# Kernel tuning notes

Measured on AMD Instinct MI355X. Metric: run time of the kernel, lower is better.

Reference implementation:

```python
import jax, jax.numpy as jnp
import numpy as np

B, S, E, H, L = 4, 512, 768, 12, 12
D = E // H
FF = 4 * E
EPS = 1e-5
SCALE = jnp.float32(768.0 ** 0.5)  # emb_size ** (1/2), applied AFTER softmax per source


def setup_inputs() -> dict:
    key = jax.random.key(0)
    ks = jax.random.split(key, 18)
    std = 0.02
    n = lambda k, shp: (jax.random.normal(k, shp, jnp.float32) * std)
    return {
        "x": jax.random.normal(ks[0], (B, S, E), jnp.float32),
        "Wqkv": n(ks[1], (L, E, 3 * E)),
        "bqkv": n(ks[2], (L, 3 * E)),
        "Wp": n(ks[3], (L, E, E)),
        "bp": n(ks[4], (L, E)),
        "W1": n(ks[5], (L, E, FF)),
        "b1": n(ks[6], (L, FF)),
        "W2": n(ks[7], (L, FF, E)),
        "b2": n(ks[8], (L, E)),
        "ln1_g": jnp.ones((L, E), jnp.float32), "ln1_b": jnp.zeros((L, E), jnp.float32),
        "ln2_g": jnp.ones((L, E), jnp.float32), "ln2_b": jnp.zeros((L, E), jnp.float32),
        "ln3_g": jnp.ones((L, E), jnp.float32), "ln3_b": jnp.zeros((L, E), jnp.float32),
        "ln4_g": jnp.ones((L, E), jnp.float32), "ln4_b": jnp.zeros((L, E), jnp.float32),
    }


def _ln(x, g, b):
    m = jnp.mean(x, axis=-1, keepdims=True)
    v = jnp.mean(jnp.square(x - m), axis=-1, keepdims=True)
    return (x - m) * jax.lax.rsqrt(v + EPS) * g + b


def _block(x, p):
    Wqkv, bqkv, Wp, bp, W1, b1, W2, b2, g1, be1, g2, be2, g3, be3, g4, be4 = p
    # --- attention branch ---
    h = _ln(x, g1, be1)
    qkv = h @ Wqkv + bqkv                      # [B,S,3E]
    qkv = qkv.reshape(B, S, H, D, 3)           # qkv is innermost factor in source rearrange
    q = jnp.transpose(qkv[..., 0], (0, 2, 1, 3))  # [B,H,S,D]
    k = jnp.transpose(qkv[..., 1], (0, 2, 1, 3))
    v = jnp.transpose(qkv[..., 2], (0, 2, 1, 3))
    energy = jnp.einsum('bhqd,bhkd->bhqk', q, k)
    att = jax.nn.softmax(energy, axis=-1) / SCALE  # NOTE: scaling AFTER softmax (faithful)
    o = jnp.einsum('bhqk,bhkd->bhqd', att, v)
    o = jnp.transpose(o, (0, 2, 1, 3)).reshape(B, S, E)
    o = o @ Wp + bp
    r1 = _ln(o, g2, be2) + x                   # first ResidualAdd (final LN inside branch)
    # --- feed-forward branch ---
    f = _ln(r1, g3, be3)
    f = jax.nn.gelu(f @ W1 + b1, approximate=False)
    f = f @ W2 + b2
    r2 = _ln(f, g4, be4) + r1                  # second ResidualAdd
    return x + r2                              # outer residual: x = x + block(x)


def reference(x, Wqkv, bqkv, Wp, bp, W1, b1, W2, b2,
              ln1_g, ln1_b, ln2_g, ln2_b, ln3_g, ln3_b, ln4_g, ln4_b):
    params = (Wqkv, bqkv, Wp, bp, W1, b1, W2, b2,
              ln1_g, ln1_b, ln2_g, ln2_b, ln3_g, ln3_b, ln4_g, ln4_b)
    out, _ = jax.lax.scan(lambda c, p: (_block(c, p), None), x, params)
    return out
```

## Files before the change

kernel.cpp:

```cpp
#include <hip/hip_runtime.h>
#include <hip/hip_bf16.h>
#include <stdint.h>

#define LAYERS 12
#define M_ROWS 2048
#define E_DIM 768
#define FF_DIM 3072
#define QKV_DIM 2304
#define SCALE_INV 0.036084391824351615f

typedef __hip_bfloat16 bf16;
typedef __attribute__((ext_vector_type(8))) __bf16 bf16x8;
typedef __attribute__((ext_vector_type(4))) float f32x4;

__device__ __forceinline__ float bf2f(bf16 v) { return __bfloat162float(v); }
__device__ __forceinline__ bf16 f2bf(float v) { return __float2bfloat16(v); }

__device__ __forceinline__ float gelu_f(float x) {
  return 0.5f * x * (1.0f + erff(x * 0.70710678118654752f));
}

__device__ __forceinline__ void async16(const bf16* g, bf16* l) {
  __builtin_amdgcn_global_load_lds(
      (const __attribute__((address_space(1))) void*)g,
      (__attribute__((address_space(3))) void*)l, 16, 0, 0);
}

__global__ __launch_bounds__(256) void transpose_k(
    const float* __restrict__ w0, const float* __restrict__ w1,
    const float* __restrict__ w2, const float* __restrict__ w3,
    bf16* __restrict__ t0, bf16* __restrict__ t1,
    bf16* __restrict__ t2, bf16* __restrict__ t3)
{
  __shared__ float T[32][33];
  int bid = blockIdx.x;
  const float* src; bf16* dst; int K, N, tile;
  if (bid < 1728)      { src = w0; dst = t0; K = 768;  N = 2304; tile = bid; }
  else if (bid < 2304) { src = w1; dst = t1; K = 768;  N = 768;  tile = bid - 1728; }
  else if (bid < 4608) { src = w2; dst = t2; K = 768;  N = 3072; tile = bid - 2304; }
  else                 { src = w3; dst = t3; K = 3072; N = 768;  tile = bid - 4608; }
  int tilesN = N >> 5;
  int tk = tile / tilesN;
  int tn = tile - tk * tilesN;
  int tx = threadIdx.x & 31, ty = threadIdx.x >> 5;
  int k0 = tk << 5, n0 = tn << 5;
#pragma unroll
  for (int i = 0; i < 4; i++)
    T[ty + i * 8][tx] = src[(size_t)(k0 + ty + i * 8) * N + n0 + tx];
  __syncthreads();
#pragma unroll
  for (int i = 0; i < 4; i++)
    dst[(size_t)(n0 + ty + i * 8) * K + k0 + tx] = f2bf(T[tx][ty + i * 8]);
}

template<int OUT_BF16, int NADD, int NPART>
__global__ __launch_bounds__(256) void ln_k(
    const float* __restrict__ in, const float* __restrict__ gamma,
    const float* __restrict__ beta, const float* __restrict__ add0,
    const float* __restrict__ add1, void* __restrict__ outp)
{
  int row = blockIdx.x, tid = threadIdx.x;
  size_t rb = (size_t)row * 768;
  float v[3]; float s = 0.f, sq = 0.f;
#pragma unroll
  for (int j = 0; j < 3; j++) {
    int c = tid + j * 256;
    float x = in[rb + c];
    if (NPART == 2) x += in[(size_t)M_ROWS * 768 + rb + c];
    v[j] = x;
    s += x; sq += x * x;
  }
#pragma unroll
  for (int off = 32; off; off >>= 1) {
    s += __shfl_xor(s, off);
    sq += __shfl_xor(sq, off);
  }
  __shared__ float red[8];
  int wv = tid >> 6;
  if ((tid & 63) == 0) { red[wv] = s; red[4 + wv] = sq; }
  __syncthreads();
  s  = red[0] + red[1] + red[2] + red[3];
  sq = red[4] + red[5] + red[6] + red[7];
  float mean = s * (1.0f / 768.0f);
  float var  = sq * (1.0f / 768.0f) - mean * mean;
  float rstd = rsqrtf(var + 1e-5f);
#pragma unroll
  for (int j = 0; j < 3; j++) {
    int c = tid + j * 256;
    float val = (v[j] - mean) * rstd * gamma[c] + beta[c];
    if (NADD >= 1) val += add0[rb + c];
    if (NADD >= 2) val += add1[rb + c];
    if (OUT_BF16) ((bf16*)outp)[rb + c] = f2bf(val);
    else          ((float*)outp)[rb + c] = val;
  }
}

template<int OUT_MODE, int NSPLIT>
__global__ __launch_bounds__(256) void gemm2_k(
    const bf16* __restrict__ A, const bf16* __restrict__ BT,
    const float* __restrict__ bias, void* __restrict__ Cout,
    bf16* __restrict__ qo, bf16* __restrict__ ko, bf16* __restrict__ vo,
    int N, int K)
{
  __shared__ __align__(16) bf16 Als[2][128 * 32];
  __shared__ __align__(16) bf16 Bls[2][64 * 32];
  int tid = threadIdx.x;
  int lane = tid & 63, w = tid >> 6;
  int l15 = lane & 15, l4 = lane >> 4;
  int Nt = N >> 6;
  int mt = blockIdx.x / Nt, ntile = blockIdx.x - mt * Nt;
  int m0 = mt << 7, n0 = ntile << 6;
  int sp = (NSPLIT > 1) ? blockIdx.y : 0;
  int Kc = K / NSPLIT;
  int kbeg = sp * Kc, kend = kbeg + Kc;
  const bf16* Ap = A + (size_t)m0 * K;
  const bf16* Bp = BT + (size_t)n0 * K;
  int ar = tid >> 2;
  int ac = (tid & 3) * 8;

  f32x4 acc[2][4] = {};

  async16(Ap + (size_t)ar * K + kbeg + ac,        &Als[0][w * 512]);
  async16(Ap + (size_t)(ar + 64) * K + kbeg + ac, &Als[0][2048 + w * 512]);
  async16(Bp + (size_t)ar * K + kbeg + ac,        &Bls[0][w * 512]);
  __syncthreads();

  int cur = 0;
  for (int k0 = kbeg; k0 < kend; k0 += 32) {
    if (k0 + 32 < kend) {
      int kn = k0 + 32;
      async16(Ap + (size_t)ar * K + kn + ac,        &Als[cur ^ 1][w * 512]);
      async16(Ap + (size_t)(ar + 64) * K + kn + ac, &Als[cur ^ 1][2048 + w * 512]);
      async16(Bp + (size_t)ar * K + kn + ac,        &Bls[cur ^ 1][w * 512]);
    }
    bf16x8 af[2], bfr[4];
#pragma unroll
    for (int i = 0; i < 2; i++)
      af[i] = *(const bf16x8*)&Als[cur][(w * 32 + i * 16 + l15) * 32 + l4 * 8];
#pragma unroll
    for (int j = 0; j < 4; j++)
      bfr[j] = *(const bf16x8*)&Bls[cur][(j * 16 + l15) * 32 + l4 * 8];
#pragma unroll
    for (int i = 0; i < 2; i++)
#pragma unroll
      for (int j = 0; j < 4; j++)
        acc[i][j] = __builtin_amdgcn_mfma_f32_16x16x32_bf16(af[i], bfr[j], acc[i][j], 0, 0, 0);
    __syncthreads();
    cur ^= 1;
  }

#pragma unroll
  for (int i = 0; i < 2; i++) {
    int mbase = m0 + w * 32 + i * 16 + (l4 << 2);
#pragma unroll
    for (int j = 0; j < 4; j++) {
      int n = n0 + j * 16 + l15;
      float bvs = (NSPLIT == 1 || sp == 0) ? bias[n] : 0.0f;
      if (OUT_MODE == 3) {
        int h = n / 192;
        int rm = n - h * 192;
        int d = rm / 3;
        int t = rm - d * 3;
#pragma unroll
        for (int rg = 0; rg < 4; rg++) {
          int m = mbase + rg;
          float val = acc[i][j][rg] + bvs;
          int b = m >> 9, sIdx = m & 511;
          int bh = b * 12 + h;
          if (t == 2)
            vo[(size_t)((bh << 6) + d) * 512 + sIdx] = f2bf(val);
          else {
            bf16* dsts = (t == 0) ? qo : ko;
            dsts[(size_t)((bh << 9) + sIdx) * 64 + d] = f2bf(val);
          }
        }
      } else {
#pragma unroll
        for (int rg = 0; rg < 4; rg++) {
          int m = mbase + rg;
          float val = acc[i][j][rg] + bvs;
          if (OUT_MODE == 0)
            ((float*)Cout)[(size_t)sp * M_ROWS * N + (size_t)m * N + n] = val;
          else if (OUT_MODE == 1)
            ((bf16*)Cout)[(size_t)m * N + n] = f2bf(val);
          else
            ((bf16*)Cout)[(size_t)m * N + n] = f2bf(gelu_f(val));
        }
      }
    }
  }
}

#define PSTR 80
__global__ __launch_bounds__(256) void attn_k(
    const bf16* __restrict__ q, const bf16* __restrict__ k,
    const bf16* __restrict__ vT, bf16* __restrict__ o)
{
  __shared__ __align__(16) bf16 Kls[64 * 64];
  __shared__ __align__(16) bf16 Vls[64 * 64];
  __shared__ __align__(16) bf16 Pls[4][16 * PSTR];
  int tid = threadIdx.x;
  int lane = tid & 63, w = tid >> 6;
  int l15 = lane & 15, l4 = lane >> 4;
  int qt = blockIdx.x & 7;
  int bh = blockIdx.x >> 3;
  size_t base = (size_t)bh * 32768;

  const bf16* qrowp = q + base + (size_t)(qt * 64 + w * 16 + l15) * 64 + l4 * 8;
  bf16x8 qf0 = *(const bf16x8*)qrowp;
  bf16x8 qf1 = *(const bf16x8*)(qrowp + 32);

  float mrow[4] = {-1e30f, -1e30f, -1e30f, -1e30f};
  float lsum[4] = {0.f, 0.f, 0.f, 0.f};
  f32x4 Oacc[4] = {};
  const f32x4 zed = {0.f, 0.f, 0.f, 0.f};
  bf16* pw = &Pls[w][0];

  for (int kt = 0; kt < 8; kt++) {
    __syncthreads();
#pragma unroll
    for (int rep = 0; rep < 2; rep++) {
      int c = tid + rep * 256;
      int row = c >> 3, col8 = (c & 7) * 8;
      *(uint4*)&Kls[row * 64 + col8] =
          *(const uint4*)(k + base + (size_t)(kt * 64 + row) * 64 + col8);
      *(uint4*)&Vls[row * 64 + col8] =
          *(const uint4*)(vT + base + (size_t)row * 512 + kt * 64 + col8);
    }
    __syncthreads();
    f32x4 e[4];
#pragma unroll
    for (int jt = 0; jt < 4; jt++) {
      bf16x8 kf0 = *(const bf16x8*)&Kls[(jt * 16 + l15) * 64 + l4 * 8];
      bf16x8 kf1 = *(const bf16x8*)&Kls[(jt * 16 + l15) * 64 + l4 * 8 + 32];
      e[jt] = __builtin_amdgcn_mfma_f32_16x16x32_bf16(qf0, kf0, zed, 0, 0, 0);
      e[jt] = __builtin_amdgcn_mfma_f32_16x16x32_bf16(qf1, kf1, e[jt], 0, 0, 0);
    }
    float al[4];
#pragma unroll
    for (int rg = 0; rg < 4; rg++) {
      float mn = fmaxf(fmaxf(e[0][rg], e[1][rg]), fmaxf(e[2][rg], e[3][rg]));
#pragma unroll
      for (int off = 1; off < 16; off <<= 1) mn = fmaxf(mn, __shfl_xor(mn, off));
      float mnew = fmaxf(mrow[rg], mn);
      al[rg] = __expf(mrow[rg] - mnew);
      mrow[rg] = mnew;
    }
    float rs[4] = {0.f, 0.f, 0.f, 0.f};
#pragma unroll
    for (int jt = 0; jt < 4; jt++)
#pragma unroll
      for (int rg = 0; rg < 4; rg++) {
        float p = __expf(e[jt][rg] - mrow[rg]);
        rs[rg] += p;
        pw[(l4 * 4 + rg) * PSTR + jt * 16 + l15] = f2bf(p);
      }
#pragma unroll
    for (int rg = 0; rg < 4; rg++) {
#pragma unroll
      for (int off = 1; off < 16; off <<= 1) rs[rg] += __shfl_xor(rs[rg], off);
      lsum[rg] = lsum[rg] * al[rg] + rs[rg];
    }
#pragma unroll
    for (int dt = 0; dt < 4; dt++)
#pragma unroll
      for (int rg = 0; rg < 4; rg++) Oacc[dt][rg] *= al[rg];
    bf16x8 pf0 = *(const bf16x8*)&pw[l15 * PSTR + l4 * 8];
    bf16x8 pf1 = *(const bf16x8*)&pw[l15 * PSTR + l4 * 8 + 32];
#pragma unroll
    for (int dt = 0; dt < 4; dt++) {
      bf16x8 vf0 = *(const bf16x8*)&Vls[(dt * 16 + l15) * 64 + l4 * 8];
      bf16x8 vf1 = *(const bf16x8*)&Vls[(dt * 16 + l15) * 64 + l4 * 8 + 32];
      Oacc[dt] = __builtin_amdgcn_mfma_f32_16x16x32_bf16(pf0, vf0, Oacc[dt], 0, 0, 0);
      Oacc[dt] = __builtin_amdgcn_mfma_f32_16x16x32_bf16(pf1, vf1, Oacc[dt], 0, 0, 0);
    }
  }
  int b = bh / 12, h = bh - b * 12;
#pragma unroll
  for (int rg = 0; rg < 4; rg++) {
    int qrow = qt * 64 + w * 16 + l4 * 4 + rg;
    float inv = SCALE_INV / lsum[rg];
    size_t rowoff = (size_t)(b * 512 + qrow) * 768 + h * 64;
#pragma unroll
    for (int dt = 0; dt < 4; dt++)
      o[rowoff + dt * 16 + l15] = f2bf(Oacc[dt][rg] * inv);
  }
}

extern "C" void kernel_launch(void* const* d_in, const int* in_sizes, int n_in,
                              void* d_out, int out_size, void* d_ws, size_t ws_size,
                              hipStream_t stream)
{
  const float* x    = (const float*)d_in[0];
  const float* Wqkv = (const float*)d_in[1];
  const float* bqkv = (const float*)d_in[2];
  const float* Wp   = (const float*)d_in[3];
  const float* bp   = (const float*)d_in[4];
  const float* W1   = (const float*)d_in[5];
  const float* b1   = (const float*)d_in[6];
  const float* W2   = (const float*)d_in[7];
  const float* b2   = (const float*)d_in[8];
  const float* g1  = (const float*)d_in[9];
  const float* be1 = (const float*)d_in[10];
  const float* g2  = (const float*)d_in[11];
  const float* be2 = (const float*)d_in[12];
  const float* g3  = (const float*)d_in[13];
  const float* be3 = (const float*)d_in[14];
  const float* g4  = (const float*)d_in[15];
  const float* be4 = (const float*)d_in[16];
  float* xout = (float*)d_out;

  char* ws = (char*)d_ws;
  size_t off = 0;
  auto alloc = [&](size_t bytes) -> char* {
    char* p = ws + off;
    off += (bytes + 255) & ~(size_t)255;
    return p;
  };
  const size_t NTOK = (size_t)M_ROWS * E_DIM;
  bf16*  qb  = (bf16*)alloc(NTOK * 2);
  bf16*  kb  = (bf16*)alloc(NTOK * 2);
  bf16*  vb  = (bf16*)alloc(NTOK * 2);
  bf16*  hb  = (bf16*)alloc(NTOK * 2);
  bf16*  ob  = (bf16*)alloc(NTOK * 2);
  bf16*  f1b = (bf16*)alloc((size_t)M_ROWS * FF_DIM * 2);
  float* tmp = (float*)alloc(NTOK * 4 * 2);
  float* r1  = (float*)alloc(NTOK * 4);
  bf16*  tq  = (bf16*)alloc((size_t)768 * 2304 * 2);
  bf16*  tp  = (bf16*)alloc((size_t)768 * 768 * 2);
  bf16*  t1  = (bf16*)alloc((size_t)768 * 3072 * 2);
  bf16*  t2  = (bf16*)alloc((size_t)3072 * 768 * 2);
  if (off > ws_size) {
    hipMemsetAsync(d_out, 0x7f, (size_t)out_size * 4, stream);
    return;
  }

  hipMemcpyAsync(d_out, x, (size_t)out_size * 4, hipMemcpyDeviceToDevice, stream);

  for (int l = 0; l < LAYERS; l++) {
    const float* wq  = Wqkv + (size_t)l * 768 * 2304;
    const float* wp_ = Wp   + (size_t)l * 768 * 768;
    const float* w1_ = W1   + (size_t)l * 768 * 3072;
    const float* w2_ = W2   + (size_t)l * 3072 * 768;

    transpose_k<<<6912, 256, 0, stream>>>(wq, wp_, w1_, w2_, tq, tp, t1, t2);

    ln_k<1, 0, 1><<<2048, 256, 0, stream>>>(xout, g1 + l * 768, be1 + l * 768,
                                            nullptr, nullptr, hb);
    gemm2_k<3, 1><<<dim3(16 * 36, 1), 256, 0, stream>>>(
        hb, tq, bqkv + (size_t)l * 2304, nullptr, qb, kb, vb, 2304, 768);
    attn_k<<<384, 256, 0, stream>>>(qb, kb, vb, ob);
    gemm2_k<0, 2><<<dim3(16 * 12, 2), 256, 0, stream>>>(
        ob, tp, bp + (size_t)l * 768, tmp, nullptr, nullptr, nullptr, 768, 768);
    ln_k<0, 1, 2><<<2048, 256, 0, stream>>>(tmp, g2 + l * 768, be2 + l * 768,
                                            xout, nullptr, r1);
    ln_k<1, 0, 1><<<2048, 256, 0, stream>>>(r1, g3 + l * 768, be3 + l * 768,
                                            nullptr, nullptr, hb);
    gemm2_k<2, 1><<<dim3(16 * 48, 1), 256, 0, stream>>>(
        hb, t1, b1 + (size_t)l * 3072, f1b, nullptr, nullptr, nullptr, 3072, 768);
    gemm2_k<0, 2><<<dim3(16 * 12, 2), 256, 0, stream>>>(
        f1b, t2, b2 + (size_t)l * 768, tmp, nullptr, nullptr, nullptr, 768, 3072);
    ln_k<0, 2, 2><<<2048, 256, 0, stream>>>(tmp, g4 + l * 768, be4 + l * 768,
                                            r1, xout, xout);
  }
}
```

Before: 1.984 ms.

## Use 128x128 GEMM tiles with XCD-aware block mapping and async attention loads

The GEMM tile grows from 128x64 to 128x128, so each wave computes a 64x64 sub-tile with 16 MFMA accumulators. This raises operand reuse per LDS load and halves the grid. Block indices are remapped so consecutive tiles land on the same XCD, which should improve L2 locality. The attention kernel now loads K/V tiles with global_load_lds async copies instead of register round-trips. The cost is fewer blocks: the Wp/W2 GEMMs get only 192 blocks, which may underfill the 256 CUs, and each thread needs more registers.

```diff
diff --git a/kernel.cpp b/kernel.cpp
--- a/kernel.cpp
+++ b/kernel.cpp
@@ -96,52 +96,62 @@
 }
 
 template<int OUT_MODE, int NSPLIT>
-__global__ __launch_bounds__(256) void gemm2_k(
+__global__ __launch_bounds__(256) void gemm3_k(
     const bf16* __restrict__ A, const bf16* __restrict__ BT,
     const float* __restrict__ bias, void* __restrict__ Cout,
     bf16* __restrict__ qo, bf16* __restrict__ ko, bf16* __restrict__ vo,
     int N, int K)
 {
   __shared__ __align__(16) bf16 Als[2][128 * 32];
-  __shared__ __align__(16) bf16 Bls[2][64 * 32];
+  __shared__ __align__(16) bf16 Bls[2][128 * 32];
   int tid = threadIdx.x;
   int lane = tid & 63, w = tid >> 6;
   int l15 = lane & 15, l4 = lane >> 4;
-  int Nt = N >> 6;
-  int mt = blockIdx.x / Nt, ntile = blockIdx.x - mt * Nt;
-  int m0 = mt << 7, n0 = ntile << 6;
+  int Nt = N >> 7;
+  int G = 16 * Nt;
+  int bid = blockIdx.x;
+  int xcd = bid & 7, jj = bid >> 3;
+  int g = xcd * (G >> 3) + jj;
+  int mt = g & 15, ntile = g >> 4;
+  int m0 = mt << 7, n0 = ntile << 7;
   int sp = (NSPLIT > 1) ? blockIdx.y : 0;
   int Kc = K / NSPLIT;
   int kbeg = sp * Kc, kend = kbeg + Kc;
-  const bf16* Ap = A + (size_t)m0 * K;
-  const bf16* Bp = BT + (size_t)n0 * K;
+  int wm = (w >> 1) * 64, wn = (w & 1) * 64;
   int ar = tid >> 2;
   int ac = (tid & 3) * 8;
 
-  f32x4 acc[2][4] = {};
-
-  async16(Ap + (size_t)ar * K + kbeg + ac,        &Als[0][w * 512]);
-  async16(Ap + (size_t)(ar + 64) * K + kbeg + ac, &Als[0][2048 + w * 512]);
-  async16(Bp + (size_t)ar * K + kbeg + ac,        &Bls[0][w * 512]);
+  const bf16* a0 = A + (size_t)(m0 + ar) * K + kbeg + ac;
+  const bf16* a1 = a0 + (size_t)64 * K;
+  const bf16* b0 = BT + (size_t)(n0 + ar) * K + kbeg + ac;
+  const bf16* b1 = b0 + (size_t)64 * K;
+
+  f32x4 acc[4][4] = {};
+
+  async16(a0, &Als[0][w * 512]);
+  async16(a1, &Als[0][2048 + w * 512]);
+  async16(b0, &Bls[0][w * 512]);
+  async16(b1, &Bls[0][2048 + w * 512]);
   __syncthreads();
 
   int cur = 0;
   for (int k0 = kbeg; k0 < kend; k0 += 32) {
     if (k0 + 32 < kend) {
-      int kn = k0 + 32;
-      async16(Ap + (size_t)ar * K + kn + ac,        &Als[cur ^ 1][w * 512]);
-      async16(Ap + (size_t)(ar + 64) * K + kn + ac, &Als[cur ^ 1][2048 + w * 512]);
-      async16(Bp + (size_t)ar * K + kn + ac,        &Bls[cur ^ 1][w * 512]);
-    }
-    bf16x8 af[2], bfr[4];
-#pragma unroll
-    for (int i = 0; i < 2; i++)
-      af[i] = *(const bf16x8*)&Als[cur][(w * 32 + i * 16 + l15) * 32 + l4 * 8];
+      a0 += 32; a1 += 32; b0 += 32; b1 += 32;
+      async16(a0, &Als[cur ^ 1][w * 512]);
+      async16(a1, &Als[cur ^ 1][2048 + w * 512]);
+      async16(b0, &Bls[cur ^ 1][w * 512]);
+      async16(b1, &Bls[cur ^ 1][2048 + w * 512]);
+    }
+    bf16x8 af[4], bfr[4];
+#pragma unroll
+    for (int i = 0; i < 4; i++)
+      af[i] = *(const bf16x8*)&Als[cur][(wm + i * 16 + l15) * 32 + l4 * 8];
 #pragma unroll
     for (int j = 0; j < 4; j++)
-      bfr[j] = *(const bf16x8*)&Bls[cur][(j * 16 + l15) * 32 + l4 * 8];
-#pragma unroll
-    for (int i = 0; i < 2; i++)
+      bfr[j] = *(const bf16x8*)&Bls[cur][(wn + j * 16 + l15) * 32 + l4 * 8];
+#pragma unroll
+    for (int i = 0; i < 4; i++)
 #pragma unroll
       for (int j = 0; j < 4; j++)
         acc[i][j] = __builtin_amdgcn_mfma_f32_16x16x32_bf16(af[i], bfr[j], acc[i][j], 0, 0, 0);
@@ -150,11 +160,11 @@
   }
 
 #pragma unroll
-  for (int i = 0; i < 2; i++) {
-    int mbase = m0 + w * 32 + i * 16 + (l4 << 2);
+  for (int i = 0; i < 4; i++) {
+    int mbase = m0 + wm + i * 16 + (l4 << 2);
 #pragma unroll
     for (int j = 0; j < 4; j++) {
-      int n = n0 + j * 16 + l15;
+      int n = n0 + wn + j * 16 + l15;
       float bvs = (NSPLIT == 1 || sp == 0) ? bias[n] : 0.0f;
       if (OUT_MODE == 3) {
         int h = n / 192;
@@ -210,6 +220,10 @@
   bf16x8 qf0 = *(const bf16x8*)qrowp;
   bf16x8 qf1 = *(const bf16x8*)(qrowp + 32);
 
+  int rr = tid >> 3, cc = (tid & 7) * 8;
+  const bf16* ksrc = k + base + (size_t)rr * 64 + cc;
+  const bf16* vsrc = vT + base + (size_t)rr * 512 + cc;
+
   float mrow[4] = {-1e30f, -1e30f, -1e30f, -1e30f};
   float lsum[4] = {0.f, 0.f, 0.f, 0.f};
   f32x4 Oacc[4] = {};
@@ -218,15 +232,10 @@
 
   for (int kt = 0; kt < 8; kt++) {
     __syncthreads();
-#pragma unroll
-    for (int rep = 0; rep < 2; rep++) {
-      int c = tid + rep * 256;
-      int row = c >> 3, col8 = (c & 7) * 8;
-      *(uint4*)&Kls[row * 64 + col8] =
-          *(const uint4*)(k + base + (size_t)(kt * 64 + row) * 64 + col8);
-      *(uint4*)&Vls[row * 64 + col8] =
-          *(const uint4*)(vT + base + (size_t)row * 512 + kt * 64 + col8);
-    }
+    async16(ksrc + (size_t)kt * 4096,        &Kls[w * 512]);
+    async16(ksrc + (size_t)kt * 4096 + 2048, &Kls[2048 + w * 512]);
+    async16(vsrc + kt * 64,                  &Vls[w * 512]);
+    async16(vsrc + kt * 64 + (size_t)32 * 512, &Vls[2048 + w * 512]);
     __syncthreads();
     f32x4 e[4];
 #pragma unroll
@@ -347,18 +356,18 @@
 
     ln_k<1, 0, 1><<<2048, 256, 0, stream>>>(xout, g1 + l * 768, be1 + l * 768,
                                             nullptr, nullptr, hb);
-    gemm2_k<3, 1><<<dim3(16 * 36, 1), 256, 0, stream>>>(
+    gemm3_k<3, 1><<<dim3(16 * 18, 1), 256, 0, stream>>>(
         hb, tq, bqkv + (size_t)l * 2304, nullptr, qb, kb, vb, 2304, 768);
     attn_k<<<384, 256, 0, stream>>>(qb, kb, vb, ob);
-    gemm2_k<0, 2><<<dim3(16 * 12, 2), 256, 0, stream>>>(
+    gemm3_k<0, 2><<<dim3(16 * 6, 2), 256, 0, stream>>>(
         ob, tp, bp + (size_t)l * 768, tmp, nullptr, nullptr, nullptr, 768, 768);
     ln_k<0, 1, 2><<<2048, 256, 0, stream>>>(tmp, g2 + l * 768, be2 + l * 768,
                                             xout, nullptr, r1);
     ln_k<1, 0, 1><<<2048, 256, 0, stream>>>(r1, g3 + l * 768, be3 + l * 768,
                                             nullptr, nullptr, hb);
-    gemm2_k<2, 1><<<dim3(16 * 48, 1), 256, 0, stream>>>(
+    gemm3_k<2, 1><<<dim3(16 * 24, 1), 256, 0, stream>>>(
         hb, t1, b1 + (size_t)l * 3072, f1b, nullptr, nullptr, nullptr, 3072, 768);
-    gemm2_k<0, 2><<<dim3(16 * 12, 2), 256, 0, stream>>>(
+    gemm3_k<0, 2><<<dim3(16 * 6, 2), 256, 0, stream>>>(
         f1b, t2, b2 + (size_t)l * 768, tmp, nullptr, nullptr, nullptr, 768, 3072);
     ln_k<0, 2, 2><<<2048, 256, 0, stream>>>(tmp, g4 + l * 768, be4 + l * 768,
                                             r1, xout, xout);
```

Result: slower. 2.195 ms (+10.6%).

## Hoist weight transposes out of layer loop, fuse adjacent LayerNorms, async attention loads

Applied to the files above, without the earlier changes.

Transposes and casts all layers' weights in a single launch up front instead of once per layer. Fuses the post-attention LayerNorm with the pre-FFN LayerNorm, and the final LayerNorm with the next layer's input LayerNorm, removing separate kernels and a re-read of the fp32 activations. Attention K/V tiles are loaded with direct global-to-LDS async loads instead of register round-trips. This uses a larger workspace for all transposed weights and relies on barriers to cover the async LDS writes.

```diff
diff --git a/kernel.cpp b/kernel.cpp
--- a/kernel.cpp
+++ b/kernel.cpp
@@ -26,19 +26,20 @@
       (__attribute__((address_space(3))) void*)l, 16, 0, 0);
 }
 
-__global__ __launch_bounds__(256) void transpose_k(
-    const float* __restrict__ w0, const float* __restrict__ w1,
-    const float* __restrict__ w2, const float* __restrict__ w3,
-    bf16* __restrict__ t0, bf16* __restrict__ t1,
-    bf16* __restrict__ t2, bf16* __restrict__ t3)
+__global__ __launch_bounds__(256) void transpose_all_k(
+    const float* __restrict__ Wqkv, const float* __restrict__ Wp,
+    const float* __restrict__ W1, const float* __restrict__ W2,
+    bf16* __restrict__ tq, bf16* __restrict__ tp,
+    bf16* __restrict__ t1, bf16* __restrict__ t2)
 {
   __shared__ float T[32][33];
+  int l = blockIdx.y;
   int bid = blockIdx.x;
   const float* src; bf16* dst; int K, N, tile;
-  if (bid < 1728)      { src = w0; dst = t0; K = 768;  N = 2304; tile = bid; }
-  else if (bid < 2304) { src = w1; dst = t1; K = 768;  N = 768;  tile = bid - 1728; }
-  else if (bid < 4608) { src = w2; dst = t2; K = 768;  N = 3072; tile = bid - 2304; }
-  else                 { src = w3; dst = t3; K = 3072; N = 768;  tile = bid - 4608; }
+  if (bid < 1728)      { src = Wqkv + (size_t)l * 768 * 2304; dst = tq + (size_t)l * 768 * 2304; K = 768;  N = 2304; tile = bid; }
+  else if (bid < 2304) { src = Wp   + (size_t)l * 768 * 768;  dst = tp + (size_t)l * 768 * 768;  K = 768;  N = 768;  tile = bid - 1728; }
+  else if (bid < 4608) { src = W1   + (size_t)l * 768 * 3072; dst = t1 + (size_t)l * 768 * 3072; K = 768;  N = 3072; tile = bid - 2304; }
+  else                 { src = W2   + (size_t)l * 3072 * 768; dst = t2 + (size_t)l * 3072 * 768; K = 3072; N = 768;  tile = bid - 4608; }
   int tilesN = N >> 5;
   int tk = tile / tilesN;
   int tn = tile - tk * tilesN;
@@ -92,6 +93,74 @@
     if (NADD >= 2) val += add1[rb + c];
     if (OUT_BF16) ((bf16*)outp)[rb + c] = f2bf(val);
     else          ((float*)outp)[rb + c] = val;
+  }
+}
+
+template<int NADD, int NPART, int WRITE2>
+__global__ __launch_bounds__(256) void lnln_k(
+    const float* __restrict__ in, const float* __restrict__ gA,
+    const float* __restrict__ bA, const float* __restrict__ add0,
+    const float* __restrict__ add1, float* __restrict__ out1,
+    const float* __restrict__ gB, const float* __restrict__ bB,
+    bf16* __restrict__ out2)
+{
+  int row = blockIdx.x, tid = threadIdx.x;
+  size_t rb = (size_t)row * 768;
+  __shared__ float red[8];
+  int wv = tid >> 6;
+
+  float v[3]; float s = 0.f, sq = 0.f;
+#pragma unroll
+  for (int j = 0; j < 3; j++) {
+    int c = tid + j * 256;
+    float x = in[rb + c];
+    if (NPART == 2) x += in[(size_t)M_ROWS * 768 + rb + c];
+    v[j] = x;
+    s += x; sq += x * x;
+  }
+#pragma unroll
+  for (int off = 32; off; off >>= 1) {
+    s += __shfl_xor(s, off);
+    sq += __shfl_xor(sq, off);
+  }
+  if ((tid & 63) == 0) { red[wv] = s; red[4 + wv] = sq; }
+  __syncthreads();
+  s  = red[0] + red[1] + red[2] + red[3];
+  sq = red[4] + red[5] + red[6] + red[7];
+  float mean = s * (1.0f / 768.0f);
+  float var  = sq * (1.0f / 768.0f) - mean * mean;
+  float rstd = rsqrtf(var + 1e-5f);
+
+  float y[3]; float s2 = 0.f, sq2 = 0.f;
+#pragma unroll
+  for (int j = 0; j < 3; j++) {
+    int c = tid + j * 256;
+    float t = (v[j] - mean) * rstd * gA[c] + bA[c];
+    if (NADD >= 1) t += add0[rb + c];
+    if (NADD >= 2) t += add1[rb + c];
+    y[j] = t;
+    out1[rb + c] = t;
+    s2 += t; sq2 += t * t;
+  }
+  if (WRITE2) {
+#pragma unroll
+    for (int off = 32; off; off >>= 1) {
+      s2 += __shfl_xor(s2, off);
+      sq2 += __shfl_xor(sq2, off);
+    }
+    __syncthreads();
+    if ((tid & 63) == 0) { red[wv] = s2; red[4 + wv] = sq2; }
+    __syncthreads();
+    s2  = red[0] + red[1] + red[2] + red[3];
+    sq2 = red[4] + red[5] + red[6] + red[7];
+    float mean2 = s2 * (1.0f / 768.0f);
+    float var2  = sq2 * (1.0f / 768.0f) - mean2 * mean2;
+    float rstd2 = rsqrtf(var2 + 1e-5f);
+#pragma unroll
+    for (int j = 0; j < 3; j++) {
+      int c = tid + j * 256;
+      out2[rb + c] = f2bf((y[j] - mean2) * rstd2 * gB[c] + bB[c]);
+    }
   }
 }
 
@@ -210,6 +279,10 @@
   bf16x8 qf0 = *(const bf16x8*)qrowp;
   bf16x8 qf1 = *(const bf16x8*)(qrowp + 32);
 
+  int rr = tid >> 3, cc = (tid & 7) * 8;
+  const bf16* ksrc = k + base + (size_t)rr * 64 + cc;
+  const bf16* vsrc = vT + base + (size_t)rr * 512 + cc;
+
   float mrow[4] = {-1e30f, -1e30f, -1e30f, -1e30f};
   float lsum[4] = {0.f, 0.f, 0.f, 0.f};
   f32x4 Oacc[4] = {};
@@ -218,15 +291,10 @@
 
   for (int kt = 0; kt < 8; kt++) {
     __syncthreads();
-#pragma unroll
-    for (int rep = 0; rep < 2; rep++) {
-      int c = tid + rep * 256;
-      int row = c >> 3, col8 = (c & 7) * 8;
-      *(uint4*)&Kls[row * 64 + col8] =
-          *(const uint4*)(k + base + (size_t)(kt * 64 + row) * 64 + col8);
-      *(uint4*)&Vls[row * 64 + col8] =
-          *(const uint4*)(vT + base + (size_t)row * 512 + kt * 64 + col8);
-    }
+    async16(ksrc + (size_t)kt * 4096,        &Kls[w * 512]);
+    async16(ksrc + (size_t)kt * 4096 + 2048, &Kls[2048 + w * 512]);
+    async16(vsrc + kt * 64,                  &Vls[w * 512]);
+    async16(vsrc + kt * 64 + (size_t)32 * 512, &Vls[2048 + w * 512]);
     __syncthreads();
     f32x4 e[4];
 #pragma unroll
@@ -326,41 +394,48 @@
   bf16*  f1b = (bf16*)alloc((size_t)M_ROWS * FF_DIM * 2);
   float* tmp = (float*)alloc(NTOK * 4 * 2);
   float* r1  = (float*)alloc(NTOK * 4);
-  bf16*  tq  = (bf16*)alloc((size_t)768 * 2304 * 2);
-  bf16*  tp  = (bf16*)alloc((size_t)768 * 768 * 2);
-  bf16*  t1  = (bf16*)alloc((size_t)768 * 3072 * 2);
-  bf16*  t2  = (bf16*)alloc((size_t)3072 * 768 * 2);
+  bf16*  tq  = (bf16*)alloc((size_t)LAYERS * 768 * 2304 * 2);
+  bf16*  tp  = (bf16*)alloc((size_t)LAYERS * 768 * 768 * 2);
+  bf16*  t1  = (bf16*)alloc((size_t)LAYERS * 768 * 3072 * 2);
+  bf16*  t2  = (bf16*)alloc((size_t)LAYERS * 3072 * 768 * 2);
   if (off > ws_size) {
     hipMemsetAsync(d_out, 0x7f, (size_t)out_size * 4, stream);
     return;
   }
 
+  transpose_all_k<<<dim3(6912, LAYERS), 256, 0, stream>>>(
+      Wqkv, Wp, W1, W2, tq, tp, t1, t2);
+
   hipMemcpyAsync(d_out, x, (size_t)out_size * 4, hipMemcpyDeviceToDevice, stream);
 
+  ln_k<1, 0, 1><<<2048, 256, 0, stream>>>(xout, g1, be1, nullptr, nullptr, hb);
+
   for (int l = 0; l < LAYERS; l++) {
-    const float* wq  = Wqkv + (size_t)l * 768 * 2304;
-    const float* wp_ = Wp   + (size_t)l * 768 * 768;
-    const float* w1_ = W1   + (size_t)l * 768 * 3072;
-    const float* w2_ = W2   + (size_t)l * 3072 * 768;
-
-    transpose_k<<<6912, 256, 0, stream>>>(wq, wp_, w1_, w2_, tq, tp, t1, t2);
-
-    ln_k<1, 0, 1><<<2048, 256, 0, stream>>>(xout, g1 + l * 768, be1 + l * 768,
-                                            nullptr, nullptr, hb);
+    const bf16* tq_l = tq + (size_t)l * 768 * 2304;
+    const bf16* tp_l = tp + (size_t)l * 768 * 768;
+    const bf16* t1_l = t1 + (size_t)l * 768 * 3072;
+    const bf16* t2_l = t2 + (size_t)l * 3072 * 768;
+
     gemm2_k<3, 1><<<dim3(16 * 36, 1), 256, 0, stream>>>(
-        hb, tq, bqkv + (size_t)l * 2304, nullptr, qb, kb, vb, 2304, 768);
+        hb, tq_l, bqkv + (size_t)l * 2304, nullptr, qb, kb, vb, 2304, 768);
     attn_k<<<384, 256, 0, stream>>>(qb, kb, vb, ob);
     gemm2_k<0, 2><<<dim3(16 * 12, 2), 256, 0, stream>>>(
-        ob, tp, bp + (size_t)l * 768, tmp, nullptr, nullptr, nullptr, 768, 768);
-    ln_k<0, 1, 2><<<2048, 256, 0, stream>>>(tmp, g2 + l * 768, be2 + l * 768,
-                                            xout, nullptr, r1);
-    ln_k<1, 0, 1><<<2048, 256, 0, stream>>>(r1, g3 + l * 768, be3 + l * 768,
-                                            nullptr, nullptr, hb);
+        ob, tp_l, bp + (size_t)l * 768, tmp, nullptr, nullptr, nullptr, 768, 768);
+    lnln_k<1, 2, 1><<<2048, 256, 0, stream>>>(
+        tmp, g2 + l * 768, be2 + l * 768, xout, nullptr, r1,
+        g3 + l * 768, be3 + l * 768, hb);
     gemm2_k<2, 1><<<dim3(16 * 48, 1), 256, 0, stream>>>(
-        hb, t1, b1 + (size_t)l * 3072, f1b, nullptr, nullptr, nullptr, 3072, 768);
+        hb, t1_l, b1 + (size_t)l * 3072, f1b, nullptr, nullptr, nullptr, 3072, 768);
     gemm2_k<0, 2><<<dim3(16 * 12, 2), 256, 0, stream>>>(
-        f1b, t2, b2 + (size_t)l * 768, tmp, nullptr, nullptr, nullptr, 768, 3072);
-    ln_k<0, 2, 2><<<2048, 256, 0, stream>>>(tmp, g4 + l * 768, be4 + l * 768,
-                                            r1, xout, xout);
-  }
-}
+        f1b, t2_l, b2 + (size_t)l * 768, tmp, nullptr, nullptr, nullptr, 768, 3072);
+    if (l + 1 < LAYERS) {
+      lnln_k<2, 2, 1><<<2048, 256, 0, stream>>>(
+          tmp, g4 + l * 768, be4 + l * 768, r1, xout, xout,
+          g1 + (l + 1) * 768, be1 + (l + 1) * 768, hb);
+    } else {
+      lnln_k<2, 2, 0><<<2048, 256, 0, stream>>>(
+          tmp, g4 + l * 768, be4 + l * 768, r1, xout, xout,
+          nullptr, nullptr, nullptr);
+    }
+  }
+}
```

After: 1.990 ms. Within noise of the previous version (+0.3%).
